# Performance work log

Hardware: AMD Instinct MI355X
Metric: run time of the kernel (lower is better)

## Reference

```python
import jax, jax.numpy as jnp
import numpy as np
import math

LEVEL_SHAPES = [(100, 152), (50, 76), (25, 38), (13, 19)]
BS, E, NH, NL, NP = 2, 256, 8, 4, 4


def _grid_init_bias(num_heads, num_levels, num_points):
    # faithful to MultiScaleDeformableAttention.init_weights sampling_offsets bias
    thetas = jnp.arange(num_heads, dtype=jnp.float32) * (2.0 * math.pi / num_heads)
    grid = jnp.stack([jnp.cos(thetas), jnp.sin(thetas)], -1)  # [H,2]
    grid = grid / jnp.max(jnp.abs(grid), axis=-1, keepdims=True)
    grid = jnp.tile(grid[:, None, None, :], (1, num_levels, num_points, 1))  # [H,L,P,2]
    scale = jnp.arange(1, num_points + 1, dtype=jnp.float32)[None, None, :, None]
    return (grid * scale).reshape(-1)


def setup_inputs() -> dict:
    key = jax.random.key(0)
    ks = jax.random.split(key, 10)
    nv = sum(h * w for h, w in LEVEL_SHAPES)  # 20197
    nq = nv
    query = jax.random.normal(ks[0], (BS, nq, E), dtype=jnp.float32)
    value = jax.random.normal(ks[1], (BS, nv, E), dtype=jnp.float32)
    reference_points = jax.random.uniform(ks[2], (BS, nq, NL, 2), dtype=jnp.float32)
    spatial_shapes = jnp.array(LEVEL_SHAPES, dtype=jnp.int32)
    sizes = [h * w for h, w in LEVEL_SHAPES]
    level_start_index = jnp.array(np.cumsum([0] + sizes)[:-1], dtype=jnp.int32)
    s = 1.0 / math.sqrt(E)
    # Linear params stored as [in, out]; y = x @ W + b
    Wv = jax.random.normal(ks[3], (E, E), dtype=jnp.float32) * s
    bv = jnp.zeros((E,), jnp.float32)
    Wso = jax.random.normal(ks[4], (E, NH * NL * NP * 2), dtype=jnp.float32) * 0.01
    bso = _grid_init_bias(NH, NL, NP)
    Waw = jax.random.normal(ks[5], (E, NH * NL * NP), dtype=jnp.float32) * 0.01
    baw = jnp.zeros((NH * NL * NP,), jnp.float32)
    Wo = jax.random.normal(ks[6], (E, E), dtype=jnp.float32) * s
    bo = jnp.zeros((E,), jnp.float32)
    return dict(query=query, value=value, reference_points=reference_points,
                spatial_shapes=spatial_shapes, level_start_index=level_start_index,
                Wv=Wv, bv=bv, Wso=Wso, bso=bso, Waw=Waw, baw=baw, Wo=Wo, bo=bo)


def _bilinear_sample(vl, loc, h, w):
    # vl: [bs, nh, h*w, d]; loc: [bs, nq, nh, P, 2] normalized in [0,1]
    # matches F.grid_sample(mode='bilinear', padding_mode='zeros', align_corners=False)
    bs, nh, _, d = vl.shape
    nq, P = loc.shape[1], loc.shape[3]
    x = loc[..., 0] * w - 0.5
    y = loc[..., 1] * h - 0.5
    x0 = jnp.floor(x).astype(jnp.int32); x1 = x0 + 1
    y0 = jnp.floor(y).astype(jnp.int32); y1 = y0 + 1
    wx1 = x - x0; wx0 = 1.0 - wx1
    wy1 = y - y0; wy0 = 1.0 - wy1

    def gather(ix, iy):
        valid = ((ix >= 0) & (ix < w) & (iy >= 0) & (iy < h)).astype(vl.dtype)
        idx = jnp.clip(iy, 0, h - 1) * w + jnp.clip(ix, 0, w - 1)  # [bs,nq,nh,P]
        idx = jnp.transpose(idx, (0, 2, 1, 3)).reshape(bs, nh, nq * P)
        g = jnp.take_along_axis(vl, idx[..., None], axis=2)  # [bs,nh,nq*P,d]
        g = g.reshape(bs, nh, nq, P, d).transpose(0, 2, 1, 3, 4)  # [bs,nq,nh,P,d]
        return g * valid[..., None]

    return (gather(x0, y0) * (wx0 * wy0)[..., None]
            + gather(x1, y0) * (wx1 * wy0)[..., None]
            + gather(x0, y1) * (wx0 * wy1)[..., None]
            + gather(x1, y1) * (wx1 * wy1)[..., None])


def reference(query, value, reference_points, spatial_shapes, level_start_index,
              Wv, bv, Wso, bso, Waw, baw, Wo, bo):
    bs, nq, e = query.shape
    nv = value.shape[1]
    nh, nl, npt = NH, NL, NP
    d = e // nh
    shapes = np.asarray(spatial_shapes)          # static level shapes
    starts = np.asarray(level_start_index)

    v = (value @ Wv + bv).reshape(bs, nv, nh, d).transpose(0, 2, 1, 3)  # [bs,nh,nv,d]
    so = (query @ Wso + bso).reshape(bs, nq, nh, nl, npt, 2)
    aw = jax.nn.softmax((query @ Waw + baw).reshape(bs, nq, nh, nl * npt), axis=-1)
    aw = aw.reshape(bs, nq, nh, nl, npt)

    # offset normalizer is (w, h) per level
    offset_norm = jnp.stack([spatial_shapes[:, 1], spatial_shapes[:, 0]], -1).astype(query.dtype)
    loc = reference_points[:, :, None, :, None, :] + so / offset_norm[None, None, None, :, None, :]

    out = jnp.zeros((bs, nq, nh, d), dtype=query.dtype)
    for l in range(nl):
        h, w = int(shapes[l, 0]), int(shapes[l, 1])
        s = int(starts[l])
        vl = v[:, :, s:s + h * w, :]                      # [bs,nh,h*w,d]
        sampled = _bilinear_sample(vl, loc[:, :, :, l], h, w)  # [bs,nq,nh,P,d]
        out = out + jnp.einsum('bqhpd,bqhp->bqhd', sampled, aw[:, :, :, l])

    out = out.reshape(bs, nq, e) @ Wo + bo
    return out + query  # identity residual (dropout in eval mode)
```

## Files before the change

### kernel.cpp

```cpp
#include <hip/hip_runtime.h>
#include <hip/hip_bf16.h>
#include <math.h>

constexpr int kBS = 2;
constexpr int kNQ = 20197;
constexpr int kNV = 20197;
constexpr int kM  = kBS * kNQ;
constexpr int kMT = 632;
constexpr int kMpad = kMT * 64;

__constant__ int cLH[4] = {100, 50, 25, 13};
__constant__ int cLW[4] = {152, 76, 38, 19};
__constant__ int cLS[4] = {0, 15200, 19000, 19950};

typedef __bf16 bf16x8 __attribute__((ext_vector_type(8)));
typedef float  f32x4  __attribute__((ext_vector_type(4)));
typedef float  f32x2  __attribute__((ext_vector_type(2)));

__device__ __forceinline__ unsigned short f2bf(float x) {
    unsigned u = __float_as_uint(x);
    return (unsigned short)((u + 0x7fffu + ((u >> 16) & 1u)) >> 16);
}
__device__ __forceinline__ unsigned pack2(float a, float b) {
    return (unsigned)f2bf(a) | ((unsigned)f2bf(b) << 16);
}
__device__ __forceinline__ float bflo(unsigned u) { return __uint_as_float(u << 16); }
__device__ __forceinline__ float bfhi(unsigned u) { return __uint_as_float(u & 0xffff0000u); }
__device__ __forceinline__ void gload_lds16(const void* g, void* s) {
    __builtin_amdgcn_global_load_lds(
        (const __attribute__((address_space(1))) void*)g,
        (__attribute__((address_space(3))) void*)s, 16, 0, 0);
}
__device__ __forceinline__ void vmwait(int n) {
    if (n == 0)      asm volatile("s_waitcnt vmcnt(0)" ::: "memory");
    else if (n == 2) asm volatile("s_waitcnt vmcnt(2)" ::: "memory");
    else             asm volatile("s_waitcnt vmcnt(4)" ::: "memory");
}

__global__ __launch_bounds__(256) void prep_w(
    const float* __restrict__ Wv, const float* __restrict__ Wso,
    const float* __restrict__ Waw, const float* __restrict__ Wo,
    const float* __restrict__ bso, const float* __restrict__ baw,
    unsigned short* __restrict__ WvT, unsigned short* __restrict__ WsoawT,
    unsigned short* __restrict__ WoT, float* __restrict__ bias384)
{
    int k = blockIdx.x * 256 + threadIdx.x;
    if (k < 65536) { int kk = k >> 8, n = k & 255; WvT[n * 256 + kk] = f2bf(Wv[k]); return; }
    k -= 65536;
    if (k < 65536) { int kk = k >> 8, n = k & 255; WsoawT[n * 256 + kk] = f2bf(Wso[k]); return; }
    k -= 65536;
    if (k < 32768) { int kk = k >> 7, n = k & 127; WsoawT[(256 + n) * 256 + kk] = f2bf(Waw[k]); return; }
    k -= 32768;
    if (k < 65536) { int kk = k >> 8, n = k & 255; WoT[n * 256 + kk] = f2bf(Wo[k]); return; }
    k -= 65536;
    if (k < 384) bias384[k] = (k < 256) ? bso[k] : baw[k - 256];
}

template<int AFP32, int CFP32>
__device__ __forceinline__ void gemm_core(
    const void* __restrict__ Av, const __hip_bfloat16* __restrict__ BT,
    const float* __restrict__ bias, const float* __restrict__ res,
    int N, int NT, void* __restrict__ Cv, int m0)
{
    __shared__ __hip_bfloat16 As[64 * 256];
    __shared__ __hip_bfloat16 Bs[4][128 * 32];

    const int t = threadIdx.x;
    const int wave = t >> 6, lane = t & 63;
    const int quad = lane >> 4, l16 = lane & 15;
    const int mw = (wave & 1) * 32, nw = (wave >> 1) * 64;
    const int NCH = NT * 8;

    auto issueB = [&](int g) {
        const int nti = g >> 3, kc = g & 7, buf = g & 3;
        #pragma unroll
        for (int j = 0; j < 2; ++j) {
            int s = j * 256 + t;
            int row = s >> 2;
            int ql = (s & 3) ^ ((row >> 1) & 3);
            gload_lds16((const char*)BT + (size_t)(nti * 128 + row) * 512
                            + kc * 64 + ql * 16,
                        (char*)&Bs[buf][0] + s * 16);
        }
    };

    if (AFP32) {
        const float* af = (const float*)Av;
        float4 fr[16];
        #pragma unroll
        for (int p = 0; p < 16; ++p) {
            int idx = p * 256 + t;
            int row = idx >> 6, col4 = idx & 63;
            fr[p] = make_float4(0.f, 0.f, 0.f, 0.f);
            if (m0 + row < kM)
                fr[p] = *(const float4*)(af + (size_t)(m0 + row) * 256 + col4 * 4);
        }
        issueB(0); issueB(1); issueB(2);
        #pragma unroll
        for (int p = 0; p < 16; ++p) {
            int idx = p * 256 + t;
            int row = idx >> 6, col4 = idx & 63;
            int ps = (col4 >> 1) ^ (row & 7);
            uint2 u = make_uint2(pack2(fr[p].x, fr[p].y), pack2(fr[p].z, fr[p].w));
            *(uint2*)(void*)((char*)As + row * 512 + ps * 16 + (col4 & 1) * 8) = u;
        }
        asm volatile("s_waitcnt lgkmcnt(0)" ::: "memory");
    } else {
        const unsigned short* ab = (const unsigned short*)Av;
        #pragma unroll
        for (int p = 0; p < 8; ++p) {
            int s = p * 256 + t;
            int row = s >> 5;
            int slog = (s & 31) ^ (row & 7);
            gload_lds16(ab + (size_t)(m0 + row) * 256 + slog * 8,
                        (char*)As + s * 16);
        }
        issueB(0); issueB(1); issueB(2);
    }

    for (int nti = 0; nti < NT; ++nti) {
        f32x4 acc[2][4] = {};
        #pragma unroll
        for (int kc = 0; kc < 8; ++kc) {
            const int g = nti * 8 + kc;
            const int left = NCH - 1 - g;
            vmwait(left >= 2 ? 4 : 2 * left);
            asm volatile("s_barrier" ::: "memory");
            if (g + 3 < NCH) issueB(g + 3);

            const int buf = g & 3;
            bf16x8 afr[2], bfr[4];
            #pragma unroll
            for (int mt = 0; mt < 2; ++mt) {
                int row = mw + mt * 16 + l16;
                int ps = (kc * 4 + quad) ^ (row & 7);
                afr[mt] = *(const bf16x8*)(const void*)
                    ((const char*)As + row * 512 + ps * 16);
            }
            #pragma unroll
            for (int nt = 0; nt < 4; ++nt) {
                int r = nw + nt * 16 + l16;
                int qp = quad ^ ((r >> 1) & 3);
                bfr[nt] = *(const bf16x8*)(const void*)
                    ((const char*)&Bs[buf][0] + r * 64 + qp * 16);
            }
            #pragma unroll
            for (int mt = 0; mt < 2; ++mt)
                #pragma unroll
                for (int nt = 0; nt < 4; ++nt)
                    acc[mt][nt] = __builtin_amdgcn_mfma_f32_16x16x32_bf16(
                        afr[mt], bfr[nt], acc[mt][nt], 0, 0, 0);
        }
        const int n0g = nti * 128;
        #pragma unroll
        for (int nt = 0; nt < 4; ++nt) {
            int col = n0g + nw + nt * 16 + l16;
            float bvv = bias[col];
            #pragma unroll
            for (int mt = 0; mt < 2; ++mt) {
                #pragma unroll
                for (int i = 0; i < 4; ++i) {
                    int row = m0 + mw + mt * 16 + quad * 4 + i;
                    if (row < kM) {
                        float val = acc[mt][nt][i] + bvv;
                        if (CFP32)
                            ((float*)Cv)[(size_t)row * N + col] =
                                val + res[(size_t)row * N + col];
                        else
                            ((unsigned short*)Cv)[(size_t)row * N + col] = f2bf(val);
                    }
                }
            }
        }
    }
}

__global__ __launch_bounds__(256, 2) void gemm_dual(
    const float* __restrict__ value, const __hip_bfloat16* __restrict__ WvT,
    const float* __restrict__ bv, unsigned short* __restrict__ v_b,
    const float* __restrict__ query, const __hip_bfloat16* __restrict__ WsoawT,
    const float* __restrict__ b384, unsigned short* __restrict__ soaw)
{
    const int m0 = blockIdx.y * 64;
    const float* A; const __hip_bfloat16* BT; const float* bias;
    unsigned short* C; int N, NT;
    if (blockIdx.x == 0) { A = value; BT = WvT;    bias = bv;   C = v_b;  N = 256; NT = 2; }
    else                 { A = query; BT = WsoawT; bias = b384; C = soaw; N = 384; NT = 3; }
    gemm_core<1, 0>(A, BT, bias, nullptr, N, NT, C, m0);
}

__global__ __launch_bounds__(256, 2) void gemm_final(
    const unsigned short* __restrict__ mid_b, const __hip_bfloat16* __restrict__ WoT,
    const float* __restrict__ bo, const float* __restrict__ query,
    float* __restrict__ out)
{
    gemm_core<0, 1>(mid_b, WoT, bo, query, 256, 2, out, blockIdx.y * 64);
}

__global__ __launch_bounds__(128) void msda_sample(
    const __hip_bfloat16* __restrict__ v,
    const __hip_bfloat16* __restrict__ soaw,
    const float* __restrict__ rp,
    __hip_bfloat16* __restrict__ mid)
{
    const int bq = blockIdx.x;
    const int b  = bq >= kNQ;
    const int t  = threadIdx.x;

    __shared__ int2 sP[128 * 5];

    {
        const int h = t >> 4, lp = t & 15, l = lp >> 2;
        unsigned sopk = *(const unsigned*)(const void*)(soaw + (size_t)bq * 384 + 2 * t);
        float logit = bflo((unsigned)*(const unsigned short*)(const void*)
                           (soaw + (size_t)bq * 384 + 256 + t));
        float2 rr = *(const float2*)(rp + (size_t)bq * 8 + l * 2);
        float sx = bflo(sopk), sy = bfhi(sopk);

        float mx = logit;
        #pragma unroll
        for (int s = 8; s >= 1; s >>= 1) mx = fmaxf(mx, __shfl_xor(mx, s, 16));
        float e = __expf(logit - mx);
        float sum = e;
        #pragma unroll
        for (int s = 8; s >= 1; s >>= 1) sum += __shfl_xor(sum, s, 16);
        float w = e / sum;

        const int ww = cLW[l], hh = cLH[l];
        const float fw = (float)ww, fh = (float)hh;
        float x = rr.x * fw + sx - 0.5f;
        float y = rr.y * fh + sy - 0.5f;
        float xf = floorf(x), yf = floorf(y);
        int x0 = (int)xf, y0 = (int)yf;
        float wx1 = x - xf, wx0 = 1.f - wx1;
        float wy1 = y - yf, wy0 = 1.f - wy1;
        bool vx0 = (x0 >= 0) & (x0 < ww);
        bool vx1 = (x0 >= -1) & (x0 + 1 < ww);
        bool vy0 = (y0 >= 0) & (y0 < hh);
        bool vy1 = (y0 >= -1) & (y0 + 1 < hh);
        int cx0 = min(max(x0, 0), ww - 1);
        int cx1 = min(max(x0 + 1, 0), ww - 1);
        int cy0 = min(max(y0, 0), hh - 1);
        int cy1 = min(max(y0 + 1, 0), hh - 1);
        const int base2 = cLS[l] * 512 + h * 64;
        sP[t * 5 + 0] = make_int2(base2 + (cy0 * ww + cx0) * 512,
                                  __float_as_int((vx0 & vy0) ? w * wx0 * wy0 : 0.f));
        sP[t * 5 + 1] = make_int2(base2 + (cy0 * ww + cx1) * 512,
                                  __float_as_int((vx1 & vy0) ? w * wx1 * wy0 : 0.f));
        sP[t * 5 + 2] = make_int2(base2 + (cy1 * ww + cx0) * 512,
                                  __float_as_int((vx0 & vy1) ? w * wx0 * wy1 : 0.f));
        sP[t * 5 + 3] = make_int2(base2 + (cy1 * ww + cx1) * 512,
                                  __float_as_int((vx1 & vy1) ? w * wx1 * wy1 : 0.f));
    }
    __syncthreads();

    const int h = t >> 4, c = (t & 15) * 2;
    const char* vb = (const char*)v + (size_t)b * ((size_t)kNV * 512);
    const unsigned cb = (unsigned)(c * 2);
    f32x2 acc = {0.f, 0.f};
    const int p0 = h * 16;
    #pragma unroll 8
    for (int pp = 0; pp < 16; ++pp) {
        const int idx = (p0 + pp) * 5;
        #pragma unroll
        for (int k2 = 0; k2 < 4; ++k2) {
            int2 pw = sP[idx + k2];
            float wgt = __int_as_float(pw.y);
            unsigned u = *(const unsigned*)(const void*)(vb + ((unsigned)pw.x + cb));
            f32x2 xy; xy.x = bflo(u); xy.y = bfhi(u);
            f32x2 w2; w2.x = wgt; w2.y = wgt;
            acc = xy * w2 + acc;
        }
    }
    *(unsigned*)(void*)(mid + (size_t)bq * 256 + h * 32 + c) = pack2(acc.x, acc.y);
}

extern "C" void kernel_launch(void* const* d_in, const int* in_sizes, int n_in,
                              void* d_out, int out_size, void* d_ws, size_t ws_size,
                              hipStream_t stream)
{
    const float* query = (const float*)d_in[0];
    const float* value = (const float*)d_in[1];
    const float* rp    = (const float*)d_in[2];
    const float* Wv  = (const float*)d_in[5];
    const float* bv  = (const float*)d_in[6];
    const float* Wso = (const float*)d_in[7];
    const float* bso = (const float*)d_in[8];
    const float* Waw = (const float*)d_in[9];
    const float* baw = (const float*)d_in[10];
    const float* Wo  = (const float*)d_in[11];
    const float* bo  = (const float*)d_in[12];

    unsigned short* v_b = (unsigned short*)d_out;

    char* p = (char*)d_ws;
    __hip_bfloat16* soaw  = (__hip_bfloat16*)p;  p += (size_t)kM * 384 * 2;
    unsigned short* mid_b = (unsigned short*)p;  p += (size_t)kMpad * 256 * 2;
    unsigned short* WvT    = (unsigned short*)p; p += 256 * 256 * 2;
    unsigned short* WsoawT = (unsigned short*)p; p += 384 * 256 * 2;
    unsigned short* WoT    = (unsigned short*)p; p += 256 * 256 * 2;
    float* bias384         = (float*)p;

    hipLaunchKernelGGL(prep_w, dim3(898), dim3(256), 0, stream,
                       Wv, Wso, Waw, Wo, bso, baw, WvT, WsoawT, WoT, bias384);

    hipLaunchKernelGGL(gemm_dual, dim3(2, kMT), dim3(256), 0, stream,
                       value, (const __hip_bfloat16*)WvT, bv, v_b,
                       query, (const __hip_bfloat16*)WsoawT, bias384,
                       (unsigned short*)soaw);

    hipLaunchKernelGGL(msda_sample, dim3(kM), dim3(128), 0, stream,
                       (const __hip_bfloat16*)v_b, soaw, rp, (__hip_bfloat16*)mid_b);

    hipLaunchKernelGGL(gemm_final, dim3(1, kMT), dim3(256), 0, stream,
                       mid_b, (const __hip_bfloat16*)WoT, bo, query, (float*)d_out);
}
```

Before: 326.0 us.

## Simplify GEMM to double-buffered B with padded A tile for higher occupancy

Replaces the 4-stage async B-tile pipeline, which used hand-tuned vmcnt waits, with a 2-buffer scheme synchronized by __syncthreads. The XOR-swizzled A tile becomes a row-padded layout, and bf16 A is now loaded through registers instead of direct-to-LDS. The smaller LDS footprint allows launch bounds to rise from 2 to 3 blocks per CU. The trade is a shallower prefetch depth and full barriers each k-step, which may expose more global-load latency in exchange for occupancy.

```diff
diff --git a/kernel.cpp b/kernel.cpp
--- a/kernel.cpp
+++ b/kernel.cpp
@@ -30,11 +30,6 @@
     __builtin_amdgcn_global_load_lds(
         (const __attribute__((address_space(1))) void*)g,
         (__attribute__((address_space(3))) void*)s, 16, 0, 0);
-}
-__device__ __forceinline__ void vmwait(int n) {
-    if (n == 0)      asm volatile("s_waitcnt vmcnt(0)" ::: "memory");
-    else if (n == 2) asm volatile("s_waitcnt vmcnt(2)" ::: "memory");
-    else             asm volatile("s_waitcnt vmcnt(4)" ::: "memory");
 }
 
 __global__ __launch_bounds__(256) void prep_w(
@@ -62,17 +57,15 @@
     const float* __restrict__ bias, const float* __restrict__ res,
     int N, int NT, void* __restrict__ Cv, int m0)
 {
-    __shared__ __hip_bfloat16 As[64 * 256];
-    __shared__ __hip_bfloat16 Bs[4][128 * 32];
+    __shared__ __hip_bfloat16 As[64 * 264];
+    __shared__ __hip_bfloat16 Bs[2][128 * 32];
 
     const int t = threadIdx.x;
     const int wave = t >> 6, lane = t & 63;
     const int quad = lane >> 4, l16 = lane & 15;
     const int mw = (wave & 1) * 32, nw = (wave >> 1) * 64;
-    const int NCH = NT * 8;
-
-    auto issueB = [&](int g) {
-        const int nti = g >> 3, kc = g & 7, buf = g & 3;
+
+    auto issueB = [&](int nti, int kc, int buf) {
         #pragma unroll
         for (int j = 0; j < 2; ++j) {
             int s = j * 256 + t;
@@ -84,65 +77,48 @@
         }
     };
 
+    issueB(0, 0, 0);
+
     if (AFP32) {
         const float* af = (const float*)Av;
-        float4 fr[16];
         #pragma unroll
         for (int p = 0; p < 16; ++p) {
             int idx = p * 256 + t;
             int row = idx >> 6, col4 = idx & 63;
-            fr[p] = make_float4(0.f, 0.f, 0.f, 0.f);
+            float4 f = make_float4(0.f, 0.f, 0.f, 0.f);
             if (m0 + row < kM)
-                fr[p] = *(const float4*)(af + (size_t)(m0 + row) * 256 + col4 * 4);
-        }
-        issueB(0); issueB(1); issueB(2);
-        #pragma unroll
-        for (int p = 0; p < 16; ++p) {
-            int idx = p * 256 + t;
-            int row = idx >> 6, col4 = idx & 63;
-            int ps = (col4 >> 1) ^ (row & 7);
-            uint2 u = make_uint2(pack2(fr[p].x, fr[p].y), pack2(fr[p].z, fr[p].w));
-            *(uint2*)(void*)((char*)As + row * 512 + ps * 16 + (col4 & 1) * 8) = u;
-        }
-        asm volatile("s_waitcnt lgkmcnt(0)" ::: "memory");
+                f = *(const float4*)(af + (size_t)(m0 + row) * 256 + col4 * 4);
+            uint2 u = make_uint2(pack2(f.x, f.y), pack2(f.z, f.w));
+            *(uint2*)(void*)&As[row * 264 + col4 * 4] = u;
+        }
     } else {
         const unsigned short* ab = (const unsigned short*)Av;
         #pragma unroll
         for (int p = 0; p < 8; ++p) {
-            int s = p * 256 + t;
-            int row = s >> 5;
-            int slog = (s & 31) ^ (row & 7);
-            gload_lds16(ab + (size_t)(m0 + row) * 256 + slog * 8,
-                        (char*)As + s * 16);
-        }
-        issueB(0); issueB(1); issueB(2);
+            int idx = p * 256 + t;
+            int row = idx >> 5, ch = idx & 31;
+            uint4 u = *(const uint4*)(ab + (size_t)(m0 + row) * 256 + ch * 8);
+            *(uint4*)(void*)&As[row * 264 + ch * 8] = u;
+        }
     }
 
     for (int nti = 0; nti < NT; ++nti) {
         f32x4 acc[2][4] = {};
-        #pragma unroll
         for (int kc = 0; kc < 8; ++kc) {
-            const int g = nti * 8 + kc;
-            const int left = NCH - 1 - g;
-            vmwait(left >= 2 ? 4 : 2 * left);
-            asm volatile("s_barrier" ::: "memory");
-            if (g + 3 < NCH) issueB(g + 3);
-
-            const int buf = g & 3;
+            __syncthreads();
+            if (kc < 7)             issueB(nti, kc + 1, (kc + 1) & 1);
+            else if (nti + 1 < NT)  issueB(nti + 1, 0, 0);
             bf16x8 afr[2], bfr[4];
             #pragma unroll
-            for (int mt = 0; mt < 2; ++mt) {
-                int row = mw + mt * 16 + l16;
-                int ps = (kc * 4 + quad) ^ (row & 7);
+            for (int mt = 0; mt < 2; ++mt)
                 afr[mt] = *(const bf16x8*)(const void*)
-                    ((const char*)As + row * 512 + ps * 16);
-            }
+                    &As[(mw + mt * 16 + l16) * 264 + kc * 32 + quad * 8];
             #pragma unroll
             for (int nt = 0; nt < 4; ++nt) {
                 int r = nw + nt * 16 + l16;
                 int qp = quad ^ ((r >> 1) & 3);
                 bfr[nt] = *(const bf16x8*)(const void*)
-                    ((const char*)&Bs[buf][0] + r * 64 + qp * 16);
+                    &Bs[kc & 1][r * 32 + qp * 8];
             }
             #pragma unroll
             for (int mt = 0; mt < 2; ++mt)
@@ -175,7 +151,7 @@
     }
 }
 
-__global__ __launch_bounds__(256, 2) void gemm_dual(
+__global__ __launch_bounds__(256, 3) void gemm_dual(
     const float* __restrict__ value, const __hip_bfloat16* __restrict__ WvT,
     const float* __restrict__ bv, unsigned short* __restrict__ v_b,
     const float* __restrict__ query, const __hip_bfloat16* __restrict__ WsoawT,
@@ -189,7 +165,7 @@
     gemm_core<1, 0>(A, BT, bias, nullptr, N, NT, C, m0);
 }
 
-__global__ __launch_bounds__(256, 2) void gemm_final(
+__global__ __launch_bounds__(256, 3) void gemm_final(
     const unsigned short* __restrict__ mid_b, const __hip_bfloat16* __restrict__ WoT,
     const float* __restrict__ bo, const float* __restrict__ query,
     float* __restrict__ out)
```

After: 303.2 us. -7.0%, faster.
